# Kernel optimization log

Hardware: AMD Instinct MI355X
Metric: run time of the kernel (lower is better)

The kernel has to match this reference:

```python
import jax, jax.numpy as jnp
import numpy as np

ROUTINGS = 3

def _squash_size1(s):
    # Faithful to squash(tensor, dim=-1) applied on a size-1 last dim:
    # squared_norm degenerates to elementwise s**2.
    sq = s * s
    return (sq / (1.0 + sq)) * s / jnp.sqrt(sq + 1e-9)

def setup_inputs() -> dict:
    key = jax.random.key(0)
    k1, k2 = jax.random.split(key)
    B, I, Din = 16, 1152, 16
    N, D = 32, 64
    inputs = jax.random.normal(k1, (B, I, Din), dtype=jnp.float32)
    W = jax.random.normal(k2, (1, N, I, D, Din), dtype=jnp.float32)
    return {"inputs": inputs, "W": W}

def reference(inputs, W):
    # inputs: [B, I, Din]; W: [1, N, I, D, Din]
    # torch: matmul(W, inputs.unsqueeze(1).unsqueeze(4)) -> [B,N,I,D,1]; drop trailing 1.
    x_hat = jnp.einsum('nidk,bik->bnid', W[0], inputs)  # [B, N, I, D]
    b = jnp.zeros_like(x_hat)                            # [B, N, I, D] (quirk: carries D axis)
    outputs = None
    for i in range(ROUTINGS):
        c = jax.nn.softmax(b, axis=2)                    # softmax over input capsules
        s = jnp.sum(c * x_hat, axis=2)                   # [B, N, D]
        outputs = _squash_size1(s)                       # elementwise squash (size-1 dim quirk)
        if i < ROUTINGS - 1:
            # (inputs_hat * outputs).sum(dim=-1) over size-1 dim == elementwise product
            b = b + x_hat * outputs[:, :, None, :]
    return outputs[..., None]                            # [B, N, D, 1] (after squeeze(2))
```

## Files before the change

### kernel.cpp

```cpp
#include <hip/hip_runtime.h>
#include <hip/hip_bf16.h>
#include <math.h>

#define B_   16
#define N_   32
#define I_   1152
#define DIN  16
#define D_   64
#define TI   16
#define IB   (I_/TI)
#define IC   16
#define BND  (B_*N_*D_)

#if __has_builtin(__builtin_amdgcn_exp2f)
#define EXP2(x) __builtin_amdgcn_exp2f(x)
#else
#define EXP2(x) exp2f(x)
#endif

#define LOG2E 1.4426950408889634f

typedef __attribute__((ext_vector_type(8))) short short8v;
typedef __attribute__((ext_vector_type(4))) float f32x4;
typedef __attribute__((ext_vector_type(4))) unsigned int u32x4;
typedef __attribute__((ext_vector_type(2))) unsigned int u32x2;

__device__ __forceinline__ float squash1(float s) {
    float sq = s * s;
    return (sq / (1.0f + sq)) * s * rsqrtf(sq + 1e-9f);
}
__device__ __forceinline__ unsigned int bfh(float v) {
    return (unsigned int)__builtin_bit_cast(unsigned short, __float2bfloat16(v));
}
__device__ __forceinline__ float bff(unsigned int hi16) {
    return __builtin_bit_cast(float, hi16 << 16);
}

#define GL16(g, l) __builtin_amdgcn_global_load_lds(                          \
    (const __attribute__((address_space(1))) void*)(g),                       \
    (__attribute__((address_space(3))) void*)(l), 16, 0, 0)

__global__ __launch_bounds__(256, 4) void k_xhat(const float* __restrict__ inp,
                                                 const float* __restrict__ W,
                                                 unsigned short* __restrict__ xh2,
                                                 float* __restrict__ part) {
    __shared__ __align__(16) unsigned short xs[4096];
    __shared__ __align__(16) float wls[2][4096];

    const int bx = blockIdx.x;
    const int n  = bx / IB;
    const int ib = bx % IB;
    const int i0 = ib * TI;
    const int t  = threadIdx.x;
    const int l  = t & 63;
    const int mt = t >> 6;
    const int ko = (l >> 4) & 1;
    const bool loHalf = (l >= 32);
    const int dd = mt * 16 + (l & 15);
    const int A_OFF   = (dd * 64 + ko * 32) ^ (((dd >> 1) & 3) << 4);
    const int lane_sw = (l * 16) ^ (((l >> 3) & 3) << 4);

    const char* Wn = (const char*)(W + (size_t)(n * I_ + i0) * 1024);

#define STAGE(c) {                                                             \
        _Pragma("unroll")                                                      \
        for (int r = 0; r < 4; ++r) {                                          \
            const char* g = Wn + (size_t)((c) * 4 + r) * 4096 + mt * 1024 + lane_sw; \
            char* ld = (char*)wls[(c) & 1] + r * 4096 + mt * 1024;             \
            GL16(g, ld);                                                       \
        } }

#define COMPQ(c) {                                                             \
        const char* wq = (const char*)wls[(c) & 1];                            \
        _Pragma("unroll")                                                      \
        for (int j = 0; j < 4; ++j) {                                          \
            const int i = (c) * 4 + j;                                         \
            f32x4 wk0 = *(const f32x4*)(wq + j * 4096 + A_OFF);                \
            f32x4 wk1 = *(const f32x4*)(wq + j * 4096 + (A_OFF ^ 16));         \
            int xaddr = ((l & 15) * 512 + i * 32 + ko * 16) ^ (((l & 15) & 7) << 4); \
            short8v bfrag = *(const short8v*)((const char*)xs + xaddr);        \
            short8v afrag;                                                     \
            _Pragma("unroll")                                                  \
            for (int q = 0; q < 8; ++q) {                                      \
                float wv = (q < 4) ? wk0[q] : wk1[q - 4];                      \
                unsigned int hi = bfh(wv);                                     \
                unsigned int lo = bfh(wv - bff(hi));                           \
                afrag[q] = (short)(loHalf ? lo : hi);                          \
            }                                                                  \
            f32x4 acc = __builtin_amdgcn_mfma_f32_16x16x32_bf16(               \
                afrag, bfrag, (f32x4){0.f, 0.f, 0.f, 0.f}, 0, 0, 0);           \
            s0v += acc;                                                        \
            pk[i * 2]     = (bfh(acc[1]) << 16) | bfh(acc[0]);                 \
            pk[i * 2 + 1] = (bfh(acc[3]) << 16) | bfh(acc[2]);                 \
        } }

    STAGE(0)

    #pragma unroll
    for (int rep = 0; rep < 2; ++rep) {
        int s   = rep * 256 + t;
        int bb  = s >> 5;
        int il  = (s >> 1) & 15;
        int sko = s & 1;
        const float* src = inp + (size_t)bb * (I_ * DIN) + (size_t)(i0 + il) * DIN + sko * 8;
        f32x4 a0 = *(const f32x4*)src;
        f32x4 a1 = *(const f32x4*)(src + 4);
        u32x4 p;
        p.x = (bfh(a0.y) << 16) | bfh(a0.x);
        p.y = (bfh(a0.w) << 16) | bfh(a0.z);
        p.z = (bfh(a1.y) << 16) | bfh(a1.x);
        p.w = (bfh(a1.w) << 16) | bfh(a1.z);
        int base = (bb * 512 + il * 32 + sko * 16) ^ ((bb & 7) << 4);
        *(u32x4*)((char*)xs + base) = p;
    }
    __syncthreads();

    unsigned int pk[TI * 2];
    f32x4 s0v = {0.f, 0.f, 0.f, 0.f};

    STAGE(1) COMPQ(0) __syncthreads();
    STAGE(2) COMPQ(1) __syncthreads();
    STAGE(3) COMPQ(2) __syncthreads();
    COMPQ(3)
#undef STAGE
#undef COMPQ

    size_t pidx = (((size_t)ib * B_ + (l & 15)) * N_ + n) * 64 + mt * 16 + (l >> 4) * 4;
    *(f32x4*)(part + pidx) = s0v;

    #pragma unroll
    for (int i = 0; i < TI; ++i) {
        u32x2 v;
        v.x = pk[i * 2];
        v.y = pk[i * 2 + 1];
        size_t off = (size_t)(n * I_ + i0 + i) * 1024 + (size_t)t * 4;
        *reinterpret_cast<u32x2*>(xh2 + off) = v;
    }
}

__global__ __launch_bounds__(256) void k_out0(const float* __restrict__ part,
                                              float* __restrict__ coef) {
    const int t = blockIdx.x * 256 + threadIdx.x;
    float s = 0.0f;
    for (int j = 0; j < IB; ++j) s += part[(size_t)j * BND + t];
    s *= (1.0f / (float)I_);
    coef[t] = squash1(s);
}

__global__ __launch_bounds__(256) void k_rpart(const unsigned short* __restrict__ xh2,
                                               const float* __restrict__ coef,
                                               float* __restrict__ part2) {
    const int bx = blockIdx.x;
    const int n  = bx >> 4;
    const int ic = bx & 15;
    const int t  = threadIdx.x;
    const int b  = t & 15;
    const int d0 = (t >> 4) * 4;

    const unsigned short* base = xh2 + ((size_t)n * I_ + (size_t)ic * (I_ / IC)) * 1024
                               + (size_t)t * 4;
    f32x4 c4 = *(const f32x4*)(coef + ((size_t)b * N_ + n) * 64 + d0);
    float c2[4] = {c4.x * LOG2E, c4.y * LOG2E, c4.z * LOG2E, c4.w * LOG2E};
    float z[4] = {0, 0, 0, 0}, a[4] = {0, 0, 0, 0};

    #pragma unroll 8
    for (int i = 0; i < I_ / IC; ++i) {
        u32x2 u = *(const u32x2*)(base + (size_t)i * 1024);
        unsigned short s4[4] = {(unsigned short)(u.x & 0xffffu), (unsigned short)(u.x >> 16),
                                (unsigned short)(u.y & 0xffffu), (unsigned short)(u.y >> 16)};
        #pragma unroll
        for (int j = 0; j < 4; ++j) {
            float x = bff(s4[j]);
            float e = EXP2(x * c2[j]);
            z[j] += e;
            a[j] = fmaf(e, x, a[j]);
        }
    }

    size_t pidx = ((((size_t)ic * N_ + n) * 16 + b) * 64 + d0) * 2;
    f32x4 v0 = {z[0], a[0], z[1], a[1]};
    f32x4 v1 = {z[2], a[2], z[3], a[3]};
    *(f32x4*)(part2 + pidx)     = v0;
    *(f32x4*)(part2 + pidx + 4) = v1;
}

__global__ __launch_bounds__(256) void k_rfin(const float* __restrict__ part2,
                                              const float* __restrict__ coefIn,
                                              float* __restrict__ outp,
                                              int final_) {
    const int gid = blockIdx.x * 256 + threadIdx.x;
    float Z = 0.0f, A = 0.0f;
    #pragma unroll
    for (int ic = 0; ic < IC; ++ic) {
        const float* p = part2 + ((size_t)ic * BND + gid) * 2;
        Z += p[0];
        A += p[1];
    }
    const int d = gid & 63, b = (gid >> 6) & 15, n = gid >> 10;
    const int ci = (b * N_ + n) * D_ + d;
    float o = squash1(A / Z);
    outp[ci] = final_ ? o : (coefIn[ci] + o);
}

extern "C" void kernel_launch(void* const* d_in, const int* in_sizes, int n_in,
                              void* d_out, int out_size, void* d_ws, size_t ws_size,
                              hipStream_t stream) {
    const float* inp = (const float*)d_in[0];
    const float* W   = (const float*)d_in[1];
    float* out = (float*)d_out;

    unsigned short* xh2 = (unsigned short*)d_ws;
    float* part  = (float*)((char*)d_ws + 75497472);
    float* part2 = (float*)((char*)d_ws + 84934656);
    float* coef  = (float*)((char*)d_ws + 89128960);

    k_xhat<<<dim3(N_ * IB), dim3(256), 0, stream>>>(inp, W, xh2, part);
    k_out0<<<dim3(BND / 256), dim3(256), 0, stream>>>(part, coef);
    k_rpart<<<dim3(N_ * IC), dim3(256), 0, stream>>>(xh2, coef, part2);
    k_rfin <<<dim3(BND / 256), dim3(256), 0, stream>>>(part2, coef, coef, 0);
    k_rpart<<<dim3(N_ * IC), dim3(256), 0, stream>>>(xh2, coef, part2);
    k_rfin <<<dim3(BND / 256), dim3(256), 0, stream>>>(part2, coef, out, 1);
}
```

Baseline: 77.62 us.

## Load all W tiles into LDS at once and use packed bf16 conversion

Replaces the double-buffered 4-stage W pipeline with a single up-front async load of all 16 W slices into a 64KB LDS buffer, which removes the intermediate barriers. The hi/lo bf16 split is now done with a truncating byte-perm for the high part and v_cvt_pk_bf16_f32 for the residual, and the output packing also uses the packed convert, cutting VALU conversion work. The larger LDS footprint and the dropped minimum-occupancy hint lower the number of blocks per CU and remove overlap between loading and compute. The truncated high part changes the rounding split, though hi+lo still represents the value.

```diff
diff --git a/kernel.cpp b/kernel.cpp
--- a/kernel.cpp
+++ b/kernel.cpp
@@ -29,23 +29,25 @@
     float sq = s * s;
     return (sq / (1.0f + sq)) * s * rsqrtf(sq + 1e-9f);
 }
-__device__ __forceinline__ unsigned int bfh(float v) {
-    return (unsigned int)__builtin_bit_cast(unsigned short, __float2bfloat16(v));
-}
 __device__ __forceinline__ float bff(unsigned int hi16) {
     return __builtin_bit_cast(float, hi16 << 16);
+}
+__device__ __forceinline__ unsigned int cvtpk(float a, float b) {
+    unsigned int r;
+    asm("v_cvt_pk_bf16_f32 %0, %1, %2" : "=v"(r) : "v"(a), "v"(b));
+    return r;
 }
 
 #define GL16(g, l) __builtin_amdgcn_global_load_lds(                          \
     (const __attribute__((address_space(1))) void*)(g),                       \
     (__attribute__((address_space(3))) void*)(l), 16, 0, 0)
 
-__global__ __launch_bounds__(256, 4) void k_xhat(const float* __restrict__ inp,
-                                                 const float* __restrict__ W,
-                                                 unsigned short* __restrict__ xh2,
-                                                 float* __restrict__ part) {
+__global__ __launch_bounds__(256) void k_xhat(const float* __restrict__ inp,
+                                              const float* __restrict__ W,
+                                              unsigned short* __restrict__ xh2,
+                                              float* __restrict__ part) {
     __shared__ __align__(16) unsigned short xs[4096];
-    __shared__ __align__(16) float wls[2][4096];
+    __shared__ __align__(16) float wls[16384];
 
     const int bx = blockIdx.x;
     const int n  = bx / IB;
@@ -62,39 +64,12 @@
 
     const char* Wn = (const char*)(W + (size_t)(n * I_ + i0) * 1024);
 
-#define STAGE(c) {                                                             \
-        _Pragma("unroll")                                                      \
-        for (int r = 0; r < 4; ++r) {                                          \
-            const char* g = Wn + (size_t)((c) * 4 + r) * 4096 + mt * 1024 + lane_sw; \
-            char* ld = (char*)wls[(c) & 1] + r * 4096 + mt * 1024;             \
-            GL16(g, ld);                                                       \
-        } }
-
-#define COMPQ(c) {                                                             \
-        const char* wq = (const char*)wls[(c) & 1];                            \
-        _Pragma("unroll")                                                      \
-        for (int j = 0; j < 4; ++j) {                                          \
-            const int i = (c) * 4 + j;                                         \
-            f32x4 wk0 = *(const f32x4*)(wq + j * 4096 + A_OFF);                \
-            f32x4 wk1 = *(const f32x4*)(wq + j * 4096 + (A_OFF ^ 16));         \
-            int xaddr = ((l & 15) * 512 + i * 32 + ko * 16) ^ (((l & 15) & 7) << 4); \
-            short8v bfrag = *(const short8v*)((const char*)xs + xaddr);        \
-            short8v afrag;                                                     \
-            _Pragma("unroll")                                                  \
-            for (int q = 0; q < 8; ++q) {                                      \
-                float wv = (q < 4) ? wk0[q] : wk1[q - 4];                      \
-                unsigned int hi = bfh(wv);                                     \
-                unsigned int lo = bfh(wv - bff(hi));                           \
-                afrag[q] = (short)(loHalf ? lo : hi);                          \
-            }                                                                  \
-            f32x4 acc = __builtin_amdgcn_mfma_f32_16x16x32_bf16(               \
-                afrag, bfrag, (f32x4){0.f, 0.f, 0.f, 0.f}, 0, 0, 0);           \
-            s0v += acc;                                                        \
-            pk[i * 2]     = (bfh(acc[1]) << 16) | bfh(acc[0]);                 \
-            pk[i * 2 + 1] = (bfh(acc[3]) << 16) | bfh(acc[2]);                 \
-        } }
-
-    STAGE(0)
+    #pragma unroll
+    for (int r = 0; r < TI; ++r) {
+        const char* g = Wn + (size_t)r * 4096 + mt * 1024 + lane_sw;
+        char* ld = (char*)wls + r * 4096 + mt * 1024;
+        GL16(g, ld);
+    }
 
     #pragma unroll
     for (int rep = 0; rep < 2; ++rep) {
@@ -106,10 +81,10 @@
         f32x4 a0 = *(const f32x4*)src;
         f32x4 a1 = *(const f32x4*)(src + 4);
         u32x4 p;
-        p.x = (bfh(a0.y) << 16) | bfh(a0.x);
-        p.y = (bfh(a0.w) << 16) | bfh(a0.z);
-        p.z = (bfh(a1.y) << 16) | bfh(a1.x);
-        p.w = (bfh(a1.w) << 16) | bfh(a1.z);
+        p.x = cvtpk(a0.x, a0.y);
+        p.y = cvtpk(a0.z, a0.w);
+        p.z = cvtpk(a1.x, a1.y);
+        p.w = cvtpk(a1.z, a1.w);
         int base = (bb * 512 + il * 32 + sko * 16) ^ ((bb & 7) << 4);
         *(u32x4*)((char*)xs + base) = p;
     }
@@ -118,12 +93,41 @@
     unsigned int pk[TI * 2];
     f32x4 s0v = {0.f, 0.f, 0.f, 0.f};
 
-    STAGE(1) COMPQ(0) __syncthreads();
-    STAGE(2) COMPQ(1) __syncthreads();
-    STAGE(3) COMPQ(2) __syncthreads();
-    COMPQ(3)
-#undef STAGE
-#undef COMPQ
+    #pragma unroll
+    for (int j = 0; j < TI; ++j) {
+        f32x4 wk0 = *(const f32x4*)((const char*)wls + j * 4096 + A_OFF);
+        f32x4 wk1 = *(const f32x4*)((const char*)wls + j * 4096 + (A_OFF ^ 16));
+        u32x4 b0 = __builtin_bit_cast(u32x4, wk0);
+        u32x4 b1 = __builtin_bit_cast(u32x4, wk1);
+        u32x4 aw;
+        if (!loHalf) {
+            aw.x = __builtin_amdgcn_perm(b0.y, b0.x, 0x07060302u);
+            aw.y = __builtin_amdgcn_perm(b0.w, b0.z, 0x07060302u);
+            aw.z = __builtin_amdgcn_perm(b1.y, b1.x, 0x07060302u);
+            aw.w = __builtin_amdgcn_perm(b1.w, b1.z, 0x07060302u);
+        } else {
+            float r0 = wk0.x - __builtin_bit_cast(float, b0.x & 0xffff0000u);
+            float r1 = wk0.y - __builtin_bit_cast(float, b0.y & 0xffff0000u);
+            float r2 = wk0.z - __builtin_bit_cast(float, b0.z & 0xffff0000u);
+            float r3 = wk0.w - __builtin_bit_cast(float, b0.w & 0xffff0000u);
+            float r4 = wk1.x - __builtin_bit_cast(float, b1.x & 0xffff0000u);
+            float r5 = wk1.y - __builtin_bit_cast(float, b1.y & 0xffff0000u);
+            float r6 = wk1.z - __builtin_bit_cast(float, b1.z & 0xffff0000u);
+            float r7 = wk1.w - __builtin_bit_cast(float, b1.w & 0xffff0000u);
+            aw.x = cvtpk(r0, r1);
+            aw.y = cvtpk(r2, r3);
+            aw.z = cvtpk(r4, r5);
+            aw.w = cvtpk(r6, r7);
+        }
+        short8v afrag = __builtin_bit_cast(short8v, aw);
+        int xaddr = ((l & 15) * 512 + j * 32 + ko * 16) ^ (((l & 15) & 7) << 4);
+        short8v bfrag = *(const short8v*)((const char*)xs + xaddr);
+        f32x4 acc = __builtin_amdgcn_mfma_f32_16x16x32_bf16(
+            afrag, bfrag, (f32x4){0.f, 0.f, 0.f, 0.f}, 0, 0, 0);
+        s0v += acc;
+        pk[j * 2]     = cvtpk(acc[0], acc[1]);
+        pk[j * 2 + 1] = cvtpk(acc[2], acc[3]);
+    }
 
     size_t pidx = (((size_t)ib * B_ + (l & 15)) * N_ + n) * 64 + mt * 16 + (l >> 4) * 4;
     *(f32x4*)(part + pidx) = s0v;
```

After: 78.97 us. Within noise of the previous version (+1.7%).
